# Kernel tuning notes

Hardware: AMD Instinct MI355X
Metric: run time of the kernel (lower is better)

The kernel has to match this reference:

```python
import jax, jax.numpy as jnp
import numpy as np


def compute_intervals(samples, L):
    """Build per-node [lower, upper) intervals for a complete binary tree.
    samples: (dim, 2^L - 1) betas, node j's beta splits its interval.
    Returns lowers, uppers: (dim, 2^L - 1), nodes in breadth-first order.
    Mirrors Tree.get_intervals: left child = [lo, lo + b*len],
    right child = [lo + b*len, lo + b*len + (1-b)*len].
    """
    dim = samples.shape[0]
    lo = jnp.zeros((dim, 1), samples.dtype)
    hi = jnp.ones((dim, 1), samples.dtype)
    lows, his = [lo], [hi]
    for l in range(L - 1):
        b = samples[:, 2**l - 1: 2**(l + 1) - 1]  # betas of level-l nodes (dim, 2^l)
        length = hi - lo
        split = lo + b * length
        right_hi = split + (1.0 - b) * length
        # children of node n are 2n+1 (left), 2n+2 (right) -> interleave
        lo = jnp.stack([lo, split], axis=-1).reshape(dim, -1)
        hi = jnp.stack([split, right_hi], axis=-1).reshape(dim, -1)
        lows.append(lo)
        his.append(hi)
    return jnp.concatenate(lows, axis=1), jnp.concatenate(his, axis=1)


def setup_inputs() -> dict:
    key = jax.random.key(0)
    k1, k2 = jax.random.split(key)
    n, dim, L = 1000000, 16, 8
    # points strictly inside (0,1) so the root interval (0,1] contains all of them
    x = jax.random.uniform(k1, (n, dim), jnp.float32, 1e-4, 1.0 - 1e-4)
    # sampled betas (stand-in for Beta(shapes,scales).rsample()), bounded away from 0/1
    samples = jax.random.uniform(k2, (dim, 2**L - 1), jnp.float32, 0.05, 0.95)
    return {"x": x, "samples": samples, "L": L}


def reference(x, samples, L):
    n, dim = x.shape
    lowers, uppers = compute_intervals(samples, L)  # (dim, n_nodes)
    loT, hiT, bT = lowers.T, uppers.T, samples.T    # (n_nodes, dim)
    d = jnp.arange(dim)[None, :]                    # (1, dim)
    idx = jnp.zeros((n, dim), jnp.int32)            # current node per (point, dim)
    log_y = jnp.zeros((n, dim), x.dtype)
    # Tree descent replaces the original's dense (n, dim, 2^L-1) containment
    # mask + nonzero + retry loop; the path visits exactly L nodes per (point, dim).
    for l in range(L):
        b = bT[idx, d]                              # (n, dim) beta at current node
        log_y = log_y + jnp.log(b)                  # prod of betas along path (in log)
        if l < L - 1:
            lo = loT[idx, d]
            hi = hiT[idx, d]
            split = lo + b * (hi - lo)
            # original containment: lower < x <= upper, so x <= split -> left child
            idx = jnp.where(x <= split, 2 * idx + 1, 2 * idx + 2)
    leaf_len = hiT[idx, d] - loT[idx, d]            # B at the leaf node
    return (log_y - jnp.log(leaf_len)).mean(axis=-1)  # (n,)
```

## Files before the change

### kernel.cpp

```cpp
#include <hip/hip_runtime.h>
#include <math.h>


constexpr int DIMS     = 16;
constexpr int NODES    = 255;
constexpr int INTERNAL = 127;
constexpr int LSTRIDE  = 128;

__global__ void build_luts(const float* __restrict__ samples,
                           float* __restrict__ split_lut,
                           float* __restrict__ value_lut)
{
#pragma clang fp contract(off)
    int t = blockIdx.x * blockDim.x + threadIdx.x;
    if (t >= DIMS * NODES) return;
    int d = t / NODES;
    int j = t - d * NODES;
    const float* s = samples + d * NODES;

    unsigned key = (unsigned)(j + 1);
    int level = 31 - __clz(key);
    float lo = 0.0f, hi = 1.0f, acc = 0.0f;
    int i = 0;
    for (int tb = level - 1; tb >= 0; --tb) {
        float b = s[i];
        acc += logf(b);
        float len = hi - lo;
        float split = lo + b * len;
        unsigned bit = (key >> tb) & 1u;
        if (bit == 0u) {
            hi = split;
        } else {
            lo = split;
            hi = split + (1.0f - b) * len;
        }
        i = 2 * i + 1 + (int)bit;
    }
    float b = s[j];
    if (j < INTERNAL) {
        float len = hi - lo;
        split_lut[d * LSTRIDE + j] = lo + b * len;
    } else {
        acc += logf(b);
        value_lut[d * LSTRIDE + (j - INTERNAL)] = acc - logf(hi - lo);
    }
}

__global__ __launch_bounds__(256) void polya_eval(
    const float* __restrict__ x,
    const float* __restrict__ split_lut,
    const float* __restrict__ value_lut,
    float* __restrict__ out,
    int n)
{
    __shared__ float s_split[DIMS * LSTRIDE];
    __shared__ float s_value[DIMS * LSTRIDE];
    for (int i = threadIdx.x; i < DIMS * LSTRIDE; i += 256) {
        s_split[i] = split_lut[i];
        s_value[i] = value_lut[i];
    }
    __syncthreads();

    const int stride = gridDim.x * 256;
    for (int p = blockIdx.x * 256 + threadIdx.x; p < n; p += stride) {
        const float4* xr = reinterpret_cast<const float4*>(x + (size_t)p * DIMS);
        float4 a = xr[0], b4 = xr[1], c = xr[2], e = xr[3];
        float xs[DIMS] = {a.x, a.y, a.z, a.w,  b4.x, b4.y, b4.z, b4.w,
                          c.x, c.y, c.z, c.w,  e.x,  e.y,  e.z,  e.w};
        float acc = 0.0f;
#pragma unroll
        for (int d = 0; d < DIMS; ++d) {
            const float xv = xs[d];
            int idx = 0;
#pragma unroll
            for (int l = 0; l < 7; ++l) {
                float sp = s_split[d * LSTRIDE + idx];
                idx = 2 * idx + 1 + (int)(xv > sp);
            }
            acc += s_value[d * LSTRIDE + (idx - INTERNAL)];
        }
        out[p] = acc * 0.0625f;
    }
}

extern "C" void kernel_launch(void* const* d_in, const int* in_sizes, int n_in,
                              void* d_out, int out_size, void* d_ws, size_t ws_size,
                              hipStream_t stream) {
    const float* x       = (const float*)d_in[0];
    const float* samples = (const float*)d_in[1];
    float* out = (float*)d_out;
    const int n = in_sizes[0] / DIMS;

    float* split_lut = (float*)d_ws;
    float* value_lut = split_lut + DIMS * LSTRIDE;

    build_luts<<<(DIMS * NODES + 255) / 256, 256, 0, stream>>>(samples, split_lut, value_lut);

    int blocks = (n + 255) / 256;
    if (blocks > 2048) blocks = 2048;
    polya_eval<<<blocks, 256, 0, stream>>>(x, split_lut, value_lut, out, n);
}
```

Measured before the change: 33.00 us.

## Pack tree levels into float4 nodes to halve LDS lookups per descent

Replaces the separate per-node split and leaf-value tables with a packed float4 layout. Each entry holds a node's split plus both children's splits, or, at the last level, the two leaf values. The descent then needs four dependent LDS loads per dimension instead of eight, at the cost of larger shared memory (about 21.7KB) and wider 16-byte loads. The grid cap of 2048 blocks is also removed, so every block handles about one point after its own LUT preload.

```diff
diff --git a/kernel.cpp b/kernel.cpp
--- a/kernel.cpp
+++ b/kernel.cpp
@@ -4,23 +4,18 @@
 
 constexpr int DIMS     = 16;
 constexpr int NODES    = 255;
-constexpr int INTERNAL = 127;
-constexpr int LSTRIDE  = 128;
 
-__global__ void build_luts(const float* __restrict__ samples,
-                           float* __restrict__ split_lut,
-                           float* __restrict__ value_lut)
-{
+constexpr int P0_OFF = 0;
+constexpr int P1_OFF = 16;
+constexpr int P2_OFF = 80;
+constexpr int P3_OFF = 336;
+constexpr int PACK_N = 1360;
+
+__device__ void node_lohi(const float* s, int j, float& lo, float& hi, float& acc) {
 #pragma clang fp contract(off)
-    int t = blockIdx.x * blockDim.x + threadIdx.x;
-    if (t >= DIMS * NODES) return;
-    int d = t / NODES;
-    int j = t - d * NODES;
-    const float* s = samples + d * NODES;
-
     unsigned key = (unsigned)(j + 1);
     int level = 31 - __clz(key);
-    float lo = 0.0f, hi = 1.0f, acc = 0.0f;
+    lo = 0.0f; hi = 1.0f; acc = 0.0f;
     int i = 0;
     for (int tb = level - 1; tb >= 0; --tb) {
         float b = s[i];
@@ -28,56 +23,92 @@
         float len = hi - lo;
         float split = lo + b * len;
         unsigned bit = (key >> tb) & 1u;
-        if (bit == 0u) {
-            hi = split;
-        } else {
-            lo = split;
-            hi = split + (1.0f - b) * len;
-        }
+        if (bit == 0u) { hi = split; }
+        else { lo = split; hi = split + (1.0f - b) * len; }
         i = 2 * i + 1 + (int)bit;
     }
-    float b = s[j];
-    if (j < INTERNAL) {
-        float len = hi - lo;
-        split_lut[d * LSTRIDE + j] = lo + b * len;
+}
+
+__device__ float node_split(const float* s, int j) {
+#pragma clang fp contract(off)
+    float lo, hi, acc;
+    node_lohi(s, j, lo, hi, acc);
+    return lo + s[j] * (hi - lo);
+}
+
+__device__ float leaf_value(const float* s, int j) {
+    float lo, hi, acc;
+    node_lohi(s, j, lo, hi, acc);
+    return acc + logf(s[j]) - logf(hi - lo);
+}
+
+__global__ void pack_build(const float* __restrict__ samples,
+                           float4* __restrict__ pack)
+{
+    int t = blockIdx.x * blockDim.x + threadIdx.x;
+    if (t >= PACK_N) return;
+    float4 e = make_float4(0.f, 0.f, 0.f, 0.f);
+    if (t < P1_OFF) {
+        const float* s = samples + t * NODES;
+        e.x = node_split(s, 0);
+        e.y = node_split(s, 1);
+        e.z = node_split(s, 2);
+    } else if (t < P2_OFF) {
+        int u = t - P1_OFF; int d = u >> 2, q = u & 3;
+        const float* s = samples + d * NODES;
+        e.x = node_split(s, 3 + q);
+        e.y = node_split(s, 7 + 2 * q);
+        e.z = node_split(s, 8 + 2 * q);
+    } else if (t < P3_OFF) {
+        int u = t - P2_OFF; int d = u >> 4, q = u & 15;
+        const float* s = samples + d * NODES;
+        e.x = node_split(s, 15 + q);
+        e.y = node_split(s, 31 + 2 * q);
+        e.z = node_split(s, 32 + 2 * q);
     } else {
-        acc += logf(b);
-        value_lut[d * LSTRIDE + (j - INTERNAL)] = acc - logf(hi - lo);
+        int u = t - P3_OFF; int d = u >> 6, q = u & 63;
+        const float* s = samples + d * NODES;
+        e.x = node_split(s, 63 + q);
+        e.y = leaf_value(s, 127 + 2 * q);
+        e.z = leaf_value(s, 128 + 2 * q);
     }
+    pack[t] = e;
 }
 
 __global__ __launch_bounds__(256) void polya_eval(
     const float* __restrict__ x,
-    const float* __restrict__ split_lut,
-    const float* __restrict__ value_lut,
+    const float4* __restrict__ pack,
     float* __restrict__ out,
     int n)
 {
-    __shared__ float s_split[DIMS * LSTRIDE];
-    __shared__ float s_value[DIMS * LSTRIDE];
-    for (int i = threadIdx.x; i < DIMS * LSTRIDE; i += 256) {
-        s_split[i] = split_lut[i];
-        s_value[i] = value_lut[i];
-    }
+    __shared__ float4 s_pack[PACK_N];
+    for (int i = threadIdx.x; i < PACK_N; i += 256) s_pack[i] = pack[i];
     __syncthreads();
 
     const int stride = gridDim.x * 256;
     for (int p = blockIdx.x * 256 + threadIdx.x; p < n; p += stride) {
         const float4* xr = reinterpret_cast<const float4*>(x + (size_t)p * DIMS);
-        float4 a = xr[0], b4 = xr[1], c = xr[2], e = xr[3];
+        float4 a = xr[0], b4 = xr[1], c = xr[2], e4 = xr[3];
         float xs[DIMS] = {a.x, a.y, a.z, a.w,  b4.x, b4.y, b4.z, b4.w,
-                          c.x, c.y, c.z, c.w,  e.x,  e.y,  e.z,  e.w};
+                          c.x, c.y, c.z, c.w,  e4.x, e4.y, e4.z, e4.w};
         float acc = 0.0f;
 #pragma unroll
         for (int d = 0; d < DIMS; ++d) {
             const float xv = xs[d];
-            int idx = 0;
-#pragma unroll
-            for (int l = 0; l < 7; ++l) {
-                float sp = s_split[d * LSTRIDE + idx];
-                idx = 2 * idx + 1 + (int)(xv > sp);
-            }
-            acc += s_value[d * LSTRIDE + (idx - INTERNAL)];
+            float4 e0 = s_pack[P0_OFF + d];
+            int b0 = (int)(xv > e0.x);
+            float s1 = b0 ? e0.z : e0.y;
+            int q = (b0 << 1) | (int)(xv > s1);
+            float4 e1 = s_pack[P1_OFF + d * 4 + q];
+            int b2 = (int)(xv > e1.x);
+            float s3 = b2 ? e1.z : e1.y;
+            q = (q << 2) | (b2 << 1) | (int)(xv > s3);
+            float4 e2 = s_pack[P2_OFF + d * 16 + q];
+            int b4i = (int)(xv > e2.x);
+            float s5 = b4i ? e2.z : e2.y;
+            q = (q << 2) | (b4i << 1) | (int)(xv > s5);
+            float4 e3 = s_pack[P3_OFF + d * 64 + q];
+            acc += (xv > e3.x) ? e3.z : e3.y;
         }
         out[p] = acc * 0.0625f;
     }
@@ -91,12 +122,10 @@
     float* out = (float*)d_out;
     const int n = in_sizes[0] / DIMS;
 
-    float* split_lut = (float*)d_ws;
-    float* value_lut = split_lut + DIMS * LSTRIDE;
+    float4* pack = (float4*)d_ws;
 
-    build_luts<<<(DIMS * NODES + 255) / 256, 256, 0, stream>>>(samples, split_lut, value_lut);
+    pack_build<<<(PACK_N + 255) / 256, 256, 0, stream>>>(samples, pack);
 
     int blocks = (n + 255) / 256;
-    if (blocks > 2048) blocks = 2048;
-    polya_eval<<<blocks, 256, 0, stream>>>(x, split_lut, value_lut, out, n);
+    polya_eval<<<blocks, 256, 0, stream>>>(x, pack, out, n);
 }
```

After: 37.58 us. +13.9%, slower.

## Replace per-dimension tree descent with sorted boundaries and uniform-grid bucket lookup

Applied to the files above, without the earlier changes.

The setup kernel now sorts the 127 split points of each dimension, builds a 1024-cell uniform grid that gives each cell a base rank and a count of boundaries inside it, and stores leaf values by rank. The eval kernel replaces the 7-step dependent shared-memory descent with one cell lookup plus a short linear scan, which cuts serial LDS latency per dimension. In exchange the shared footprint grows to 48KB, which limits occupancy, the scan loop length varies with the data, and the setup kernel does O(127^2) rank work on only 16 blocks. The grid size is also changed to 1536 blocks.

```diff
diff --git a/kernel.cpp b/kernel.cpp
--- a/kernel.cpp
+++ b/kernel.cpp
@@ -2,25 +2,20 @@
 #include <math.h>
 
 
-constexpr int DIMS     = 16;
-constexpr int NODES    = 255;
-constexpr int INTERNAL = 127;
-constexpr int LSTRIDE  = 128;
+constexpr int DIMS  = 16;
+constexpr int NODES = 255;
+constexpr int GRIDC = 1024;
 
-__global__ void build_luts(const float* __restrict__ samples,
-                           float* __restrict__ split_lut,
-                           float* __restrict__ value_lut)
-{
+constexpr int BND_OFF  = 0;
+constexpr int VAL_OFF  = 2048;
+constexpr int CELL_OFF = 4096;
+constexpr int WS_U32   = 12288;
+
+__device__ void node_lohi(const float* s, int j, float& lo, float& hi, float& acc) {
 #pragma clang fp contract(off)
-    int t = blockIdx.x * blockDim.x + threadIdx.x;
-    if (t >= DIMS * NODES) return;
-    int d = t / NODES;
-    int j = t - d * NODES;
-    const float* s = samples + d * NODES;
-
     unsigned key = (unsigned)(j + 1);
     int level = 31 - __clz(key);
-    float lo = 0.0f, hi = 1.0f, acc = 0.0f;
+    lo = 0.0f; hi = 1.0f; acc = 0.0f;
     int i = 0;
     for (int tb = level - 1; tb >= 0; --tb) {
         float b = s[i];
@@ -28,56 +23,110 @@
         float len = hi - lo;
         float split = lo + b * len;
         unsigned bit = (key >> tb) & 1u;
-        if (bit == 0u) {
-            hi = split;
-        } else {
-            lo = split;
-            hi = split + (1.0f - b) * len;
-        }
+        if (bit == 0u) { hi = split; }
+        else { lo = split; hi = split + (1.0f - b) * len; }
         i = 2 * i + 1 + (int)bit;
     }
-    float b = s[j];
-    if (j < INTERNAL) {
-        float len = hi - lo;
-        split_lut[d * LSTRIDE + j] = lo + b * len;
-    } else {
-        acc += logf(b);
-        value_lut[d * LSTRIDE + (j - INTERNAL)] = acc - logf(hi - lo);
+}
+
+__device__ float node_split(const float* s, int j) {
+#pragma clang fp contract(off)
+    float lo, hi, acc;
+    node_lohi(s, j, lo, hi, acc);
+    return lo + s[j] * (hi - lo);
+}
+
+__global__ __launch_bounds__(256) void build_tables(
+    const float* __restrict__ samples,
+    unsigned* __restrict__ ws)
+{
+    const int d   = blockIdx.x;
+    const int tid = threadIdx.x;
+    const float* s = samples + d * NODES;
+
+    float* bnd_g = (float*)(ws + BND_OFF) + d * 128;
+    float* val_g = (float*)(ws + VAL_OFF) + d * 128;
+    unsigned short* cell_g = (unsigned short*)(ws + CELL_OFF) + d * GRIDC;
+
+    __shared__ float raw[127];
+    __shared__ float srt[128];
+
+    if (tid < 127) raw[tid] = node_split(s, tid);
+    if (tid == 127) srt[127] = INFINITY;
+    __syncthreads();
+
+    if (tid < 127) {
+        float v = raw[tid];
+        int rank = 0;
+        for (int j = 0; j < 127; ++j) {
+            float w = raw[j];
+            rank += (int)((w < v) || (w == v && j < tid));
+        }
+        srt[rank] = v;
+    }
+    __syncthreads();
+
+    if (tid < 128) bnd_g[tid] = srt[tid];
+
+    for (int c = tid; c < GRIDC; c += 256) {
+        int base = 0, k = 0;
+        for (int j = 0; j < 127; ++j) {
+            int cb = (int)(srt[j] * 1024.0f);
+            base += (int)(cb < c);
+            k    += (int)(cb == c);
+        }
+        cell_g[c] = (unsigned short)((base << 8) | k);
+    }
+
+    if (tid < 128) {
+        int j = 127 + tid;
+        float lo, hi, acc;
+        node_lohi(s, j, lo, hi, acc);
+        if (hi > lo) {
+            float v = acc + logf(s[j]) - logf(hi - lo);
+            int rank = 0;
+            for (int i = 0; i < 127; ++i) rank += (int)(srt[i] <= lo);
+            val_g[rank] = v;
+        }
     }
 }
 
 __global__ __launch_bounds__(256) void polya_eval(
     const float* __restrict__ x,
-    const float* __restrict__ split_lut,
-    const float* __restrict__ value_lut,
+    const unsigned* __restrict__ ws,
     float* __restrict__ out,
     int n)
 {
-    __shared__ float s_split[DIMS * LSTRIDE];
-    __shared__ float s_value[DIMS * LSTRIDE];
-    for (int i = threadIdx.x; i < DIMS * LSTRIDE; i += 256) {
-        s_split[i] = split_lut[i];
-        s_value[i] = value_lut[i];
+    __shared__ unsigned s_mem[WS_U32];
+    {
+        const uint4* src = (const uint4*)ws;
+        uint4* dst = (uint4*)s_mem;
+        for (int i = threadIdx.x; i < WS_U32 / 4; i += 256) dst[i] = src[i];
     }
     __syncthreads();
+    const float* s_bnd = (const float*)(s_mem + BND_OFF);
+    const float* s_val = (const float*)(s_mem + VAL_OFF);
+    const unsigned short* s_cell = (const unsigned short*)(s_mem + CELL_OFF);
 
     const int stride = gridDim.x * 256;
     for (int p = blockIdx.x * 256 + threadIdx.x; p < n; p += stride) {
         const float4* xr = reinterpret_cast<const float4*>(x + (size_t)p * DIMS);
-        float4 a = xr[0], b4 = xr[1], c = xr[2], e = xr[3];
+        float4 a = xr[0], b4 = xr[1], c4 = xr[2], e4 = xr[3];
         float xs[DIMS] = {a.x, a.y, a.z, a.w,  b4.x, b4.y, b4.z, b4.w,
-                          c.x, c.y, c.z, c.w,  e.x,  e.y,  e.z,  e.w};
+                          c4.x, c4.y, c4.z, c4.w,  e4.x, e4.y, e4.z, e4.w};
         float acc = 0.0f;
 #pragma unroll
         for (int d = 0; d < DIMS; ++d) {
             const float xv = xs[d];
-            int idx = 0;
-#pragma unroll
-            for (int l = 0; l < 7; ++l) {
-                float sp = s_split[d * LSTRIDE + idx];
-                idx = 2 * idx + 1 + (int)(xv > sp);
-            }
-            acc += s_value[d * LSTRIDE + (idx - INTERNAL)];
+            const int c = (int)(xv * 1024.0f);
+            const unsigned u = s_cell[(d << 10) + c];
+            const int base = (int)(u >> 8);
+            const int k = (int)(u & 255u);
+            const float* bd = s_bnd + (d << 7);
+            int r = base + (int)(xv > bd[base]);
+            for (int j = 1; j < k; ++j)
+                r += (int)(xv > bd[base + j]);
+            acc += s_val[(d << 7) + r];
         }
         out[p] = acc * 0.0625f;
     }
@@ -90,13 +139,9 @@
     const float* samples = (const float*)d_in[1];
     float* out = (float*)d_out;
     const int n = in_sizes[0] / DIMS;
+    unsigned* ws = (unsigned*)d_ws;
 
-    float* split_lut = (float*)d_ws;
-    float* value_lut = split_lut + DIMS * LSTRIDE;
+    build_tables<<<DIMS, 256, 0, stream>>>(samples, ws);
 
-    build_luts<<<(DIMS * NODES + 255) / 256, 256, 0, stream>>>(samples, split_lut, value_lut);
-
-    int blocks = (n + 255) / 256;
-    if (blocks > 2048) blocks = 2048;
-    polya_eval<<<blocks, 256, 0, stream>>>(x, split_lut, value_lut, out, n);
+    polya_eval<<<1536, 256, 0, stream>>>(x, ws, out, n);
 }
```

Measured after the change: 51.62 us. 1.56x slower.

## Keep top tree levels in registers and store LUT levels contiguously

Applied to the files above, without the earlier changes.

Splits the split-point table into per-level arrays and resolves the first three tree levels per dimension with register-held splits and selects instead of LDS lookups. The remaining four levels plus the leaf values are read from a packed shared-memory table indexed by the path bits. It also sets a launch-bounds occupancy hint and halves the grid cap. Holding 112 split values in registers per thread raises register pressure and could lower occupancy, and the kernel is likely limited by memory bandwidth on the 64 MB input anyway.

```diff
diff --git a/kernel.cpp b/kernel.cpp
--- a/kernel.cpp
+++ b/kernel.cpp
@@ -2,14 +2,38 @@
 #include <math.h>
 
 
-constexpr int DIMS     = 16;
-constexpr int NODES    = 255;
-constexpr int INTERNAL = 127;
-constexpr int LSTRIDE  = 128;
+constexpr int DIMS  = 16;
+constexpr int NODES = 255;
+
+constexpr int TOP_OFF = 0;
+constexpr int L3_OFF  = 128;
+constexpr int L4_OFF  = 256;
+constexpr int L5_OFF  = 512;
+constexpr int L6_OFF  = 1024;
+constexpr int VAL_OFF = 2048;
+constexpr int WS_F    = 4096;
+constexpr int LDS_F   = WS_F - L3_OFF;
+
+__device__ void node_lohi(const float* s, int j, float& lo, float& hi, float& acc) {
+#pragma clang fp contract(off)
+    unsigned key = (unsigned)(j + 1);
+    int level = 31 - __clz(key);
+    lo = 0.0f; hi = 1.0f; acc = 0.0f;
+    int i = 0;
+    for (int tb = level - 1; tb >= 0; --tb) {
+        float b = s[i];
+        acc += logf(b);
+        float len = hi - lo;
+        float split = lo + b * len;
+        unsigned bit = (key >> tb) & 1u;
+        if (bit == 0u) { hi = split; }
+        else { lo = split; hi = split + (1.0f - b) * len; }
+        i = 2 * i + 1 + (int)bit;
+    }
+}
 
 __global__ void build_luts(const float* __restrict__ samples,
-                           float* __restrict__ split_lut,
-                           float* __restrict__ value_lut)
+                           float* __restrict__ ws)
 {
 #pragma clang fp contract(off)
     int t = blockIdx.x * blockDim.x + threadIdx.x;
@@ -18,66 +42,64 @@
     int j = t - d * NODES;
     const float* s = samples + d * NODES;
 
-    unsigned key = (unsigned)(j + 1);
-    int level = 31 - __clz(key);
-    float lo = 0.0f, hi = 1.0f, acc = 0.0f;
-    int i = 0;
-    for (int tb = level - 1; tb >= 0; --tb) {
-        float b = s[i];
-        acc += logf(b);
-        float len = hi - lo;
-        float split = lo + b * len;
-        unsigned bit = (key >> tb) & 1u;
-        if (bit == 0u) {
-            hi = split;
-        } else {
-            lo = split;
-            hi = split + (1.0f - b) * len;
-        }
-        i = 2 * i + 1 + (int)bit;
-    }
+    float lo, hi, acc;
+    node_lohi(s, j, lo, hi, acc);
     float b = s[j];
-    if (j < INTERNAL) {
-        float len = hi - lo;
-        split_lut[d * LSTRIDE + j] = lo + b * len;
+    if (j < 127) {
+        float split = lo + b * (hi - lo);
+        if (j < 7)        ws[TOP_OFF + d * 8   + j]        = split;
+        else if (j < 15)  ws[L3_OFF  + d * 8   + (j - 7)]  = split;
+        else if (j < 31)  ws[L4_OFF  + d * 16  + (j - 15)] = split;
+        else if (j < 63)  ws[L5_OFF  + d * 32  + (j - 31)] = split;
+        else              ws[L6_OFF  + d * 64  + (j - 63)] = split;
     } else {
-        acc += logf(b);
-        value_lut[d * LSTRIDE + (j - INTERNAL)] = acc - logf(hi - lo);
+        float v = acc + logf(b) - logf(hi - lo);
+        ws[VAL_OFF + d * 128 + (j - 127)] = v;
     }
 }
 
-__global__ __launch_bounds__(256) void polya_eval(
+__global__ __launch_bounds__(256, 4) void polya_eval(
     const float* __restrict__ x,
-    const float* __restrict__ split_lut,
-    const float* __restrict__ value_lut,
+    const float* __restrict__ tbl,
     float* __restrict__ out,
     int n)
 {
-    __shared__ float s_split[DIMS * LSTRIDE];
-    __shared__ float s_value[DIMS * LSTRIDE];
-    for (int i = threadIdx.x; i < DIMS * LSTRIDE; i += 256) {
-        s_split[i] = split_lut[i];
-        s_value[i] = value_lut[i];
+    __shared__ float s_t[LDS_F];
+    for (int i = threadIdx.x; i < LDS_F; i += 256) s_t[i] = tbl[L3_OFF + i];
+    __syncthreads();
+
+    float S0[DIMS], S1[DIMS], S2[DIMS];
+    float C0[DIMS], C1[DIMS], C2[DIMS], C3[DIMS];
+#pragma unroll
+    for (int d = 0; d < DIMS; ++d) {
+        const float* t = tbl + TOP_OFF + d * 8;
+        S0[d] = t[0]; S1[d] = t[1]; S2[d] = t[2];
+        C0[d] = t[3]; C1[d] = t[4]; C2[d] = t[5]; C3[d] = t[6];
     }
-    __syncthreads();
 
     const int stride = gridDim.x * 256;
     for (int p = blockIdx.x * 256 + threadIdx.x; p < n; p += stride) {
         const float4* xr = reinterpret_cast<const float4*>(x + (size_t)p * DIMS);
-        float4 a = xr[0], b4 = xr[1], c = xr[2], e = xr[3];
+        float4 a = xr[0], b4 = xr[1], c4 = xr[2], e4 = xr[3];
         float xs[DIMS] = {a.x, a.y, a.z, a.w,  b4.x, b4.y, b4.z, b4.w,
-                          c.x, c.y, c.z, c.w,  e.x,  e.y,  e.z,  e.w};
+                          c4.x, c4.y, c4.z, c4.w,  e4.x, e4.y, e4.z, e4.w};
         float acc = 0.0f;
 #pragma unroll
         for (int d = 0; d < DIMS; ++d) {
             const float xv = xs[d];
-            int idx = 0;
-#pragma unroll
-            for (int l = 0; l < 7; ++l) {
-                float sp = s_split[d * LSTRIDE + idx];
-                idx = 2 * idx + 1 + (int)(xv > sp);
-            }
-            acc += s_value[d * LSTRIDE + (idx - INTERNAL)];
+            const int b0 = (int)(xv > S0[d]);
+            const float m1 = b0 ? S2[d] : S1[d];
+            const int b1 = (int)(xv > m1);
+            const float ta = b1 ? C1[d] : C0[d];
+            const float tb = b1 ? C3[d] : C2[d];
+            const float m2 = b0 ? tb : ta;
+            const int b2 = (int)(xv > m2);
+            int q = (b0 << 2) | (b1 << 1) | b2;
+            q = (q << 1) | (int)(xv > s_t[        d * 8   + q]);
+            q = (q << 1) | (int)(xv > s_t[128  +  d * 16  + q]);
+            q = (q << 1) | (int)(xv > s_t[384  +  d * 32  + q]);
+            q = (q << 1) | (int)(xv > s_t[896  +  d * 64  + q]);
+            acc += s_t[1920 + d * 128 + q];
         }
         out[p] = acc * 0.0625f;
     }
@@ -90,13 +112,11 @@
     const float* samples = (const float*)d_in[1];
     float* out = (float*)d_out;
     const int n = in_sizes[0] / DIMS;
+    float* ws = (float*)d_ws;
 
-    float* split_lut = (float*)d_ws;
-    float* value_lut = split_lut + DIMS * LSTRIDE;
-
-    build_luts<<<(DIMS * NODES + 255) / 256, 256, 0, stream>>>(samples, split_lut, value_lut);
+    build_luts<<<(DIMS * NODES + 255) / 256, 256, 0, stream>>>(samples, ws);
 
     int blocks = (n + 255) / 256;
-    if (blocks > 2048) blocks = 2048;
-    polya_eval<<<blocks, 256, 0, stream>>>(x, split_lut, value_lut, out, n);
+    if (blocks > 1024) blocks = 1024;
+    polya_eval<<<blocks, 256, 0, stream>>>(x, ws, out, n);
 }
```

New measurement: 50.88 us. 54.2% more time.
